# Kernel tuning notes

Measured on AMD Instinct MI355X. Metric: run time of the kernel, lower is better.

Reference implementation:

```python
import jax, jax.numpy as jnp
import numpy as np

# ---- static config (from init_kwargs) ----
SCALE = 1.0
N = 16384
DX = SCALE / N          # grid step = cutoff / 2
CUTOFF = 2.0 * DX
SQRT2 = float(np.sqrt(2.0))


def circ_conv(x, w):
    """Circularly-padded 1D cross-correlation (torch Conv1d, padding_mode='circular').
    x: [B, Cin, N], w: [Cout, Cin, K] (K odd). Returns [B, Cout, N]."""
    p = w.shape[-1] // 2
    xp = jnp.concatenate([x[..., -p:], x, x[..., :p]], axis=-1)
    return jax.lax.conv_general_dilated(
        xp, w, window_strides=(1,), padding='VALID',
        dimension_numbers=('NCH', 'OIH', 'NCH'))


def setup_inputs() -> dict:
    key = jax.random.key(0)
    ks = jax.random.split(key, 8)
    x = jax.random.normal(ks[0], (1024, 1, N), dtype=jnp.float32)
    # centered 4th-order accurate first-derivative stencil (acc=4), scaled by 1/dx
    deriv = np.array([1.0 / 12.0, -2.0 / 3.0, 0.0, 2.0 / 3.0, -1.0 / 12.0],
                     dtype=np.float32) / DX
    deriv_w = jnp.asarray(deriv).reshape(1, 1, 5)
    # discrete Box filter of width cutoff = 2*dx (trapezoidal weights)
    filt_w = jnp.asarray(np.array([0.25, 0.5, 0.25], dtype=np.float32)).reshape(1, 1, 3)
    # BasicNet(in=2, mid=[6,3], out=1, k=5, bias=True): kaiming-ish scaled init
    def conv_init(k, cout, cin, ks_):
        return jax.random.normal(k, (cout, cin, ks_), dtype=jnp.float32) / np.sqrt(cin * ks_)
    W1 = conv_init(ks[1], 6, 2, 5); b1 = jax.random.normal(ks[2], (6,), dtype=jnp.float32) * 0.01
    W2 = conv_init(ks[3], 3, 6, 5); b2 = jax.random.normal(ks[4], (3,), dtype=jnp.float32) * 0.01
    W3 = conv_init(ks[5], 1, 3, 5); b3 = jax.random.normal(ks[6], (1,), dtype=jnp.float32) * 0.01
    return {"x": x, "deriv_w": deriv_w, "filt_w": filt_w,
            "W1": W1, "b1": b1, "W2": W2, "b2": b2, "W3": W3, "b3": b3}


def reference(x, deriv_w, filt_w, W1, b1, W2, b2, W3, b3):
    xdiff = circ_conv(x, deriv_w)                                # [B,1,N]
    feat = jnp.concatenate([xdiff, x - circ_conv(x, filt_w)], axis=1)  # [B,2,N]
    h = jax.nn.elu(circ_conv(feat, W1) + b1[None, :, None])      # [B,6,N]
    h = jax.nn.elu(circ_conv(h, W2) + b2[None, :, None])         # [B,3,N]
    cs = jax.nn.elu(circ_conv(h, W3) + b3[None, :, None])        # [B,1,N]
    cs = jnp.clip(cs, 0.0, 1.0)                                  # Hardtanh(bounds)
    y = (cs * CUTOFF) ** 2 * jnp.abs(xdiff) * xdiff
    return circ_conv(SQRT2 * y, deriv_w)
```

## Files before the change

### kernel.cpp

```cpp
#include <hip/hip_runtime.h>
#include <math.h>

#define NN 16384
#define T 512

typedef float f2 __attribute__((ext_vector_type(2)));

__device__ __forceinline__ f2 elu2(f2 v) {
    f2 e;
    e.x = __expf(v.x);
    e.y = __expf(v.y);
    const f2 zero = (f2)0.0f;
    return __builtin_elementwise_max(v, zero)
         + __builtin_elementwise_min(e - 1.0f, zero);
}

__global__ __launch_bounds__(256, 8)
void smag_al(const float* __restrict__ x,
             const float* __restrict__ dw,
             const float* __restrict__ fw,
             const float* __restrict__ W1, const float* __restrict__ b1,
             const float* __restrict__ W2, const float* __restrict__ b2,
             const float* __restrict__ W3, const float* __restrict__ b3,
             float* __restrict__ out)
{
    const int blk = blockIdx.x & 31;
    const int row = blockIdx.x >> 5;
    const int tb  = blk * T;
    const int tid = threadIdx.x;
    const float* __restrict__ xr = x   + (size_t)row * NN;
    float* __restrict__ outr     = out + (size_t)row * NN;

    __shared__ __align__(16) float sm[5232];
    float* const sxd = sm;
    float* const sh1 = sm + 528;
    float* const sy  = sm + 528;
    float* const sh2 = sm + 3672;
    float* const sx  = sm + 3672;
    float* const sf1 = sm + 4208;

    {
        f2 v = *(const f2*)(xr + tb + 2 * tid);
        *(f2*)(sx + 2 * tid + 12) = v;
        if (tid < 20) {
            int p = (tid < 10) ? (tid - 10) : (T + tid - 10);
            sx[p + 12] = xr[(tb + p + NN) & (NN - 1)];
        }
    }

    const float d0 = dw[0], d1 = dw[1], d2 = dw[2], d3 = dw[3], d4 = dw[4];
    const float g0 = fw[0], g1 = fw[1], g2 = fw[2];
    __syncthreads();

    auto S1 = [&](int p) {
        f2 L0 = *(f2*)(sx + p + 10);
        f2 L1 = *(f2*)(sx + p + 12);
        f2 L2 = *(f2*)(sx + p + 14);
        f2 a12 = {L0.y, L1.x};
        f2 a34 = {L1.y, L2.x};
        f2 xd = L0 * d0 + a12 * d1 + L1 * d2 + a34 * d3 + L2 * d4;
        f2 f1 = L1 - (a12 * g0 + L1 * g1 + a34 * g2);
        *(f2*)(sxd + p + 8) = xd;
        *(f2*)(sf1 + p + 8) = f1;
    };
    S1(2 * tid - 8);
    if (tid < 8) S1(504 + 2 * tid);
    __syncthreads();

    auto S2 = [&](int p) {
        f2 X0 = *(f2*)(sxd + p + 6);
        f2 X1 = *(f2*)(sxd + p + 8);
        f2 X2 = *(f2*)(sxd + p + 10);
        f2 F0 = *(f2*)(sf1 + p + 6);
        f2 F1 = *(f2*)(sf1 + p + 8);
        f2 F2 = *(f2*)(sf1 + p + 10);
        f2 xa[5] = {X0, {X0.y, X1.x}, X1, {X1.y, X2.x}, X2};
        f2 fa[5] = {F0, {F0.y, F1.x}, F1, {F1.y, F2.x}, F2};
        #pragma unroll
        for (int c = 0; c < 6; ++c) {
            f2 a = (f2)b1[c];
            #pragma unroll
            for (int k = 0; k < 5; ++k)
                a = a + xa[k] * W1[c * 10 + k] + fa[k] * W1[c * 10 + 5 + k];
            *(f2*)(sh1 + c * 524 + p + 6) = elu2(a);
        }
    };
    S2(2 * tid - 6);
    if (tid < 6) S2(506 + 2 * tid);
    __syncthreads();

    auto S3 = [&](int p) {
        f2 acc0 = (f2)b2[0], acc1 = (f2)b2[1], acc2 = (f2)b2[2];
        #pragma unroll
        for (int ci = 0; ci < 6; ++ci) {
            const float* hb = sh1 + ci * 524 + p + 4;
            f2 H0 = *(f2*)(hb);
            f2 H1 = *(f2*)(hb + 2);
            f2 H2 = *(f2*)(hb + 4);
            f2 ha[5] = {H0, {H0.y, H1.x}, H1, {H1.y, H2.x}, H2};
            #pragma unroll
            for (int k = 0; k < 5; ++k) {
                acc0 = acc0 + ha[k] * W2[0 * 30 + ci * 5 + k];
                acc1 = acc1 + ha[k] * W2[1 * 30 + ci * 5 + k];
                acc2 = acc2 + ha[k] * W2[2 * 30 + ci * 5 + k];
            }
        }
        *(f2*)(sh2 + 0 * 520 + p + 4) = elu2(acc0);
        *(f2*)(sh2 + 1 * 520 + p + 4) = elu2(acc1);
        *(f2*)(sh2 + 2 * 520 + p + 4) = elu2(acc2);
    };
    S3(2 * tid - 4);
    if (tid < 4) S3(508 + 2 * tid);
    __syncthreads();

    const float B3v = b3[0];
    const float K = 1.41421356237309515f * (float)(2.0/16384.0) * (float)(2.0/16384.0);
    auto S4 = [&](int p) {
        f2 a = (f2)B3v;
        #pragma unroll
        for (int ci = 0; ci < 3; ++ci) {
            const float* hb = sh2 + ci * 520 + p + 2;
            f2 H0 = *(f2*)(hb);
            f2 H1 = *(f2*)(hb + 2);
            f2 H2 = *(f2*)(hb + 4);
            f2 ha1 = {H0.y, H1.x};
            f2 ha3 = {H1.y, H2.x};
            a = a + H0 * W3[ci * 5 + 0] + ha1 * W3[ci * 5 + 1] + H1 * W3[ci * 5 + 2]
                  + ha3 * W3[ci * 5 + 3] + H2 * W3[ci * 5 + 4];
        }
        f2 xd = *(f2*)(sxd + p + 8);
        f2 cs = __builtin_elementwise_min(__builtin_elementwise_max(a, (f2)0.0f), (f2)1.0f);
        f2 axd = __builtin_elementwise_abs(xd);
        f2 y = (cs * cs) * (axd * xd) * K;
        *(f2*)(sy + p + 2) = y;
    };
    S4(2 * tid - 2);
    if (tid < 2) S4(510 + 2 * tid);
    __syncthreads();

    {
        const int p = 2 * tid;
        f2 Y0 = *(f2*)(sy + p);
        f2 Y1 = *(f2*)(sy + p + 2);
        f2 Y2 = *(f2*)(sy + p + 4);
        f2 a12 = {Y0.y, Y1.x};
        f2 a34 = {Y1.y, Y2.x};
        f2 o = Y0 * d0 + a12 * d1 + Y1 * d2 + a34 * d3 + Y2 * d4;
        *(f2*)(outr + tb + p) = o;
    }
}

extern "C" void kernel_launch(void* const* d_in, const int* in_sizes, int n_in,
                              void* d_out, int out_size, void* d_ws, size_t ws_size,
                              hipStream_t stream) {
    const float* x  = (const float*)d_in[0];
    const float* dw = (const float*)d_in[1];
    const float* fw = (const float*)d_in[2];
    const float* W1 = (const float*)d_in[3];
    const float* b1 = (const float*)d_in[4];
    const float* W2 = (const float*)d_in[5];
    const float* b2 = (const float*)d_in[6];
    const float* W3 = (const float*)d_in[7];
    const float* b3 = (const float*)d_in[8];
    float* out = (float*)d_out;

    const int B = 1024;
    dim3 grid(B * (NN / T));
    dim3 block(256);
    hipLaunchKernelGGL(smag_al, grid, block, 0, stream,
                       x, dw, fw, W1, b1, W2, b2, W3, b3, out);
}
```

Baseline: 116.2 us.

## Fold derivative and filter stencils into a 9-tap first conv layer

A small setup kernel composes the derivative stencil, the box filter and the first layer's weights into effective 9-tap weights per output channel. The main kernel then computes layer 1 directly from x read from global memory, dropping the shared-memory staging of x, xdiff and the filtered signal along with two barriers. xdiff for the final product is kept in registers. This trades shared-memory traffic and syncs for redundant overlapping global loads, and adds a tiny extra kernel launch.

```diff
diff --git a/kernel.cpp b/kernel.cpp
--- a/kernel.cpp
+++ b/kernel.cpp
@@ -15,11 +15,36 @@
          + __builtin_elementwise_min(e - 1.0f, zero);
 }
 
+__global__ void smag_setup(const float* __restrict__ dw,
+                           const float* __restrict__ fw,
+                           const float* __restrict__ W1,
+                           float* __restrict__ cw)
+{
+    const int t = threadIdx.x;
+    if (t < 54) {
+        const int c = t / 9;
+        const int m = (t % 9) - 4;
+        float acc = 0.0f;
+        #pragma unroll
+        for (int k = 0; k < 5; ++k) {
+            int j = m + 4 - k;
+            if (j >= 0 && j <= 4) acc += W1[c * 10 + k] * dw[j];
+        }
+        if (m >= -2 && m <= 2) acc += W1[c * 10 + 5 + (m + 2)];
+        #pragma unroll
+        for (int i = 0; i < 3; ++i) {
+            int k = m + 3 - i;
+            if (k >= 0 && k <= 4) acc -= fw[i] * W1[c * 10 + 5 + k];
+        }
+        cw[t] = acc;
+    }
+}
+
 __global__ __launch_bounds__(256, 8)
-void smag_al(const float* __restrict__ x,
+void smag_c9(const float* __restrict__ x,
              const float* __restrict__ dw,
-             const float* __restrict__ fw,
-             const float* __restrict__ W1, const float* __restrict__ b1,
+             const float* __restrict__ cw,
+             const float* __restrict__ b1,
              const float* __restrict__ W2, const float* __restrict__ b2,
              const float* __restrict__ W3, const float* __restrict__ b3,
              float* __restrict__ out)
@@ -31,69 +56,44 @@
     const float* __restrict__ xr = x   + (size_t)row * NN;
     float* __restrict__ outr     = out + (size_t)row * NN;
 
-    __shared__ __align__(16) float sm[5232];
-    float* const sxd = sm;
-    float* const sh1 = sm + 528;
-    float* const sy  = sm + 528;
-    float* const sh2 = sm + 3672;
-    float* const sx  = sm + 3672;
-    float* const sf1 = sm + 4208;
-
-    {
-        f2 v = *(const f2*)(xr + tb + 2 * tid);
-        *(f2*)(sx + 2 * tid + 12) = v;
-        if (tid < 20) {
-            int p = (tid < 10) ? (tid - 10) : (T + tid - 10);
-            sx[p + 12] = xr[(tb + p + NN) & (NN - 1)];
-        }
-    }
+    __shared__ __align__(16) float sm[4704];
+    float* const sh1 = sm;
+    float* const sy  = sm;
+    float* const sh2 = sm + 3144;
 
     const float d0 = dw[0], d1 = dw[1], d2 = dw[2], d3 = dw[3], d4 = dw[4];
-    const float g0 = fw[0], g1 = fw[1], g2 = fw[2];
-    __syncthreads();
 
-    auto S1 = [&](int p) {
-        f2 L0 = *(f2*)(sx + p + 10);
-        f2 L1 = *(f2*)(sx + p + 12);
-        f2 L2 = *(f2*)(sx + p + 14);
-        f2 a12 = {L0.y, L1.x};
-        f2 a34 = {L1.y, L2.x};
-        f2 xd = L0 * d0 + a12 * d1 + L1 * d2 + a34 * d3 + L2 * d4;
-        f2 f1 = L1 - (a12 * g0 + L1 * g1 + a34 * g2);
-        *(f2*)(sxd + p + 8) = xd;
-        *(f2*)(sf1 + p + 8) = f1;
-    };
-    S1(2 * tid - 8);
-    if (tid < 8) S1(504 + 2 * tid);
-    __syncthreads();
-
-    auto S2 = [&](int p) {
-        f2 X0 = *(f2*)(sxd + p + 6);
-        f2 X1 = *(f2*)(sxd + p + 8);
-        f2 X2 = *(f2*)(sxd + p + 10);
-        f2 F0 = *(f2*)(sf1 + p + 6);
-        f2 F1 = *(f2*)(sf1 + p + 8);
-        f2 F2 = *(f2*)(sf1 + p + 10);
-        f2 xa[5] = {X0, {X0.y, X1.x}, X1, {X1.y, X2.x}, X2};
-        f2 fa[5] = {F0, {F0.y, F1.x}, F1, {F1.y, F2.x}, F2};
+    f2 xd_main, xd_tail;
+    auto S2p = [&](int p, f2& xd_out) {
+        f2 G[6];
+        #pragma unroll
+        for (int t = 0; t < 6; ++t) {
+            int g = (tb + p - 4 + 2 * t + NN) & (NN - 1);
+            G[t] = *(const f2*)(xr + g);
+        }
+        f2 w9[9] = {G[0], {G[0].y, G[1].x}, G[1], {G[1].y, G[2].x}, G[2],
+                    {G[2].y, G[3].x}, G[3], {G[3].y, G[4].x}, G[4]};
         #pragma unroll
         for (int c = 0; c < 6; ++c) {
             f2 a = (f2)b1[c];
             #pragma unroll
-            for (int k = 0; k < 5; ++k)
-                a = a + xa[k] * W1[c * 10 + k] + fa[k] * W1[c * 10 + 5 + k];
+            for (int m = 0; m < 9; ++m)
+                a = a + w9[m] * cw[c * 9 + m];
             *(f2*)(sh1 + c * 524 + p + 6) = elu2(a);
         }
+        f2 a12 = {G[3].y, G[4].x};
+        f2 a34 = {G[4].y, G[5].x};
+        xd_out = G[3] * d0 + a12 * d1 + G[4] * d2 + a34 * d3 + G[5] * d4;
     };
-    S2(2 * tid - 6);
-    if (tid < 6) S2(506 + 2 * tid);
+    S2p(2 * tid - 6, xd_main);
+    if (tid < 6) S2p(506 + 2 * tid, xd_tail);
     __syncthreads();
 
-    auto S3 = [&](int p) {
+    auto S3 = [&](int q) {
         f2 acc0 = (f2)b2[0], acc1 = (f2)b2[1], acc2 = (f2)b2[2];
         #pragma unroll
         for (int ci = 0; ci < 6; ++ci) {
-            const float* hb = sh1 + ci * 524 + p + 4;
+            const float* hb = sh1 + ci * 524 + q + 4;
             f2 H0 = *(f2*)(hb);
             f2 H1 = *(f2*)(hb + 2);
             f2 H2 = *(f2*)(hb + 4);
@@ -105,9 +105,9 @@
                 acc2 = acc2 + ha[k] * W2[2 * 30 + ci * 5 + k];
             }
         }
-        *(f2*)(sh2 + 0 * 520 + p + 4) = elu2(acc0);
-        *(f2*)(sh2 + 1 * 520 + p + 4) = elu2(acc1);
-        *(f2*)(sh2 + 2 * 520 + p + 4) = elu2(acc2);
+        *(f2*)(sh2 + 0 * 520 + q + 4) = elu2(acc0);
+        *(f2*)(sh2 + 1 * 520 + q + 4) = elu2(acc1);
+        *(f2*)(sh2 + 2 * 520 + q + 4) = elu2(acc2);
     };
     S3(2 * tid - 4);
     if (tid < 4) S3(508 + 2 * tid);
@@ -115,11 +115,11 @@
 
     const float B3v = b3[0];
     const float K = 1.41421356237309515f * (float)(2.0/16384.0) * (float)(2.0/16384.0);
-    auto S4 = [&](int p) {
+    auto S4 = [&](int q, f2 xd) {
         f2 a = (f2)B3v;
         #pragma unroll
         for (int ci = 0; ci < 3; ++ci) {
-            const float* hb = sh2 + ci * 520 + p + 2;
+            const float* hb = sh2 + ci * 520 + q + 2;
             f2 H0 = *(f2*)(hb);
             f2 H1 = *(f2*)(hb + 2);
             f2 H2 = *(f2*)(hb + 4);
@@ -128,14 +128,13 @@
             a = a + H0 * W3[ci * 5 + 0] + ha1 * W3[ci * 5 + 1] + H1 * W3[ci * 5 + 2]
                   + ha3 * W3[ci * 5 + 3] + H2 * W3[ci * 5 + 4];
         }
-        f2 xd = *(f2*)(sxd + p + 8);
         f2 cs = __builtin_elementwise_min(__builtin_elementwise_max(a, (f2)0.0f), (f2)1.0f);
         f2 axd = __builtin_elementwise_abs(xd);
         f2 y = (cs * cs) * (axd * xd) * K;
-        *(f2*)(sy + p + 2) = y;
+        *(f2*)(sy + q + 2) = y;
     };
-    S4(2 * tid - 2);
-    if (tid < 2) S4(510 + 2 * tid);
+    S4(2 * tid - 2, xd_main);
+    if (tid < 2) S4(510 + 2 * tid, xd_tail);
     __syncthreads();
 
     {
@@ -163,10 +162,13 @@
     const float* W3 = (const float*)d_in[7];
     const float* b3 = (const float*)d_in[8];
     float* out = (float*)d_out;
+    float* cw  = (float*)d_ws;
+
+    hipLaunchKernelGGL(smag_setup, dim3(1), dim3(64), 0, stream, dw, fw, W1, cw);
 
     const int B = 1024;
     dim3 grid(B * (NN / T));
     dim3 block(256);
-    hipLaunchKernelGGL(smag_al, grid, block, 0, stream,
-                       x, dw, fw, W1, b1, W2, b2, W3, b3, out);
+    hipLaunchKernelGGL(smag_c9, grid, block, 0, stream,
+                       x, dw, cw, b1, W2, b2, W3, b3, out);
 }
```

After: 111.5 us. 1.04x faster.
